# Kernel tuning notes

Hardware: AMD Instinct MI355X
Metric: run time of the kernel (lower is better)

Reference implementation:

```python
import jax, jax.numpy as jnp
import numpy as np

EMB = 2048
NH = 16
HD = EMB // NH  # 128

def setup_inputs() -> dict:
    key = jax.random.key(0)
    kx, kw1, kw2 = jax.random.split(key, 3)
    T = 4096
    x = jax.random.normal(kx, (T, EMB), dtype=jnp.float32)
    lim_in = 1.0 / np.sqrt(EMB)
    # input_proj: Linear(EMB, 3*EMB, use_bias=False), weight shape (out, in)
    W_in = jax.random.uniform(kw1, (3 * EMB, EMB), minval=-lim_in, maxval=lim_in, dtype=jnp.float32)
    W_out = jax.random.uniform(kw2, (EMB, EMB), minval=-lim_in, maxval=lim_in, dtype=jnp.float32)
    return {"x": x, "W_in": W_in, "W_out": W_out}

def reference(x, W_in, W_out):
    T = x.shape[0]
    norm = 1.0 / np.sqrt(HD)
    qkv = x @ W_in.T                         # [T, 3E]
    Q, K, V = jnp.split(qkv, 3, axis=-1)     # each [T, E]
    Q = Q.reshape(T, NH, HD).transpose(1, 0, 2)  # [nh, T, hd]
    K = K.reshape(T, NH, HD).transpose(1, 0, 2)
    V = V.reshape(T, NH, HD).transpose(1, 0, 2)
    A = jnp.einsum('htd,hsd->hts', Q, K) * norm  # [nh, T, T]
    mask = jnp.tri(T, dtype=bool)                # causal: keep lower triangle
    A = jnp.where(mask, A, -jnp.inf)
    P = jax.nn.softmax(A, axis=-1)
    y = jnp.einsum('hts,hsd->htd', P, V)         # [nh, T, hd]
    y = y.transpose(1, 0, 2).reshape(T, EMB)     # concat heads
    return y @ W_out.T
```

## Files before the change

### kernel.cpp

```cpp
#include <hip/hip_runtime.h>
#include <hip/hip_bf16.h>
#include <cstddef>


typedef __attribute__((ext_vector_type(8))) short short8;
typedef __attribute__((ext_vector_type(4))) float f32x4;

#define MFMA16(a, b, c) __builtin_amdgcn_mfma_f32_16x16x32_bf16((a), (b), (c), 0, 0, 0)

#define GLOAD_LDS16(gptr, lptr)                                                          \
  __builtin_amdgcn_global_load_lds((const __attribute__((address_space(1))) void*)(gptr), \
                                   (__attribute__((address_space(3))) void*)(lptr), 16, 0, 0)

__device__ __forceinline__ short f2bf(float f) {
  __hip_bfloat16 h = __float2bfloat16(f);
  return *reinterpret_cast<short*>(&h);
}

__device__ __forceinline__ void storeC(float* p, float v) { *p = v; }
__device__ __forceinline__ void storeC(short* p, float v) { *p = f2bf(v); }

__global__ void cvt_bf16(const float* __restrict__ in, short* __restrict__ out, long n) {
  long i = ((long)blockIdx.x * 256 + threadIdx.x) * 8;
  if (i >= n) return;
  f32x4 a = *(const f32x4*)(in + i);
  f32x4 b = *(const f32x4*)(in + i + 4);
  short8 o;
  o[0] = f2bf(a[0]); o[1] = f2bf(a[1]); o[2] = f2bf(a[2]); o[3] = f2bf(a[3]);
  o[4] = f2bf(b[0]); o[5] = f2bf(b[1]); o[6] = f2bf(b[2]); o[7] = f2bf(b[3]);
  *(short8*)(out + i) = o;
}

template <typename CT>
__global__ __launch_bounds__(256, 2)
void gemm_bt(const short* __restrict__ A, const short* __restrict__ B,
             CT* __restrict__ C, int M, int N, int K, float cscale, int nscale) {
  __shared__ short As[128 * 32];
  __shared__ short Bs[128 * 32];
  const int tid = threadIdx.x;
  const int wave = tid >> 6, lane = tid & 63;
  const int g = lane >> 4, fr = lane & 15;
  const int wr = (wave >> 1) * 64, wc = (wave & 1) * 64;
  const int bm = blockIdx.y * 128, bn = blockIdx.x * 128;

  f32x4 acc[4][4] = {};

  for (int k0 = 0; k0 < K; k0 += 32) {
    __syncthreads();
#pragma unroll
    for (int i = 0; i < 2; ++i) {
      int Ci = i * 256 + tid;
      int row = Ci >> 2, c = Ci & 3;
      int sc = c ^ (row & 3);
      GLOAD_LDS16(A + (size_t)(bm + row) * K + k0 + sc * 8, As + Ci * 8);
      GLOAD_LDS16(B + (size_t)(bn + row) * K + k0 + sc * 8, Bs + Ci * 8);
    }
    __syncthreads();

    short8 af[4], bfr[4];
#pragma unroll
    for (int m = 0; m < 4; ++m) {
      int row = wr + m * 16 + fr;
      int off = (g * 8) ^ ((row & 3) * 8);
      af[m] = *(const short8*)(As + row * 32 + off);
    }
#pragma unroll
    for (int n = 0; n < 4; ++n) {
      int row = wc + n * 16 + fr;
      int off = (g * 8) ^ ((row & 3) * 8);
      bfr[n] = *(const short8*)(Bs + row * 32 + off);
    }
#pragma unroll
    for (int m = 0; m < 4; ++m)
#pragma unroll
      for (int n = 0; n < 4; ++n)
        acc[m][n] = MFMA16(af[m], bfr[n], acc[m][n]);
  }

#pragma unroll
  for (int m = 0; m < 4; ++m) {
#pragma unroll
    for (int r = 0; r < 4; ++r) {
      size_t row = (size_t)(bm + wr + m * 16 + g * 4 + r);
      CT* cp = C + row * N + bn + wc + fr;
#pragma unroll
      for (int n = 0; n < 4; ++n) {
        float sc = (bn + wc + n * 16 + fr < nscale) ? cscale : 1.0f;
        storeC(cp + n * 16, acc[m][n][r] * sc);
      }
    }
  }
}

__global__ __launch_bounds__(256, 4)
void vtrans(const short* __restrict__ qkv, short* __restrict__ vtg) {
  __shared__ short L[128 * 64];
  const int tid = threadIdx.x;
  const int tb = blockIdx.x * 64;
  const int h = blockIdx.y;
#pragma unroll
  for (int i = 0; i < 4; ++i) {
    int Ci = i * 256 + tid, tok = Ci >> 4, c = Ci & 15, f0 = c * 8;
    short8 v = *(const short8*)(qkv + (size_t)(tb + tok) * 6144 + 4096 + h * 128 + f0);
#pragma unroll
    for (int j = 0; j < 8; ++j) {
      int f = f0 + j;
      L[f * 64 + (tok ^ ((((f & 7) ^ ((f >> 3) & 7)) << 3)))] = v[j];
    }
  }
  __syncthreads();
  const int f = tid >> 1, half = (tid & 1) * 32;
  const int s_in = ((f & 7) ^ ((f >> 3) & 7)) << 3;
  const int s_out = (f & 7) << 3;
#pragma unroll
  for (int j2 = 0; j2 < 4; ++j2) {
    int t0 = half + j2 * 8;
    short8 v = *(const short8*)(&L[f * 64 + (t0 ^ s_in)]);
    *(short8*)(vtg + (size_t)(h * 128 + f) * 4096 + tb + (t0 ^ s_out)) = v;
  }
}

__global__ __launch_bounds__(256, 1)
void attn_fwd(const short* __restrict__ qkv, const short* __restrict__ vtg,
              short* __restrict__ y) {
  __shared__ short Ks[2][64 * 128];
  __shared__ short Vt[2][128 * 64];
  __shared__ short Ps[4][32 * 72];
  const int tid = threadIdx.x;
  const int wave = tid >> 6, lane = tid & 63;
  const int g = lane >> 4, fr = lane & 15;

  const int wgid = blockIdx.x;
  const int slot = wgid >> 3;
  const int h = ((wgid & 7) << 1) | (slot >> 4);
  const int pair = slot & 15;

  short* Pw = Ps[wave];

  short8 onesf;
#pragma unroll
  for (int j = 0; j < 8; ++j) onesf[j] = (short)0x3F80;

#pragma unroll 1
  for (int phase = 0; phase < 2; ++phase) {
    const int xb = phase ? (31 - pair) : pair;
    const int qw = xb * 128 + wave * 32;
    const int ntiles = 2 * xb + 2;

    short8 qf[2][4];
#pragma unroll
    for (int mi = 0; mi < 2; ++mi) {
      const short* Qp = qkv + (size_t)(qw + mi * 16 + fr) * 6144 + h * 128;
#pragma unroll
      for (int kk = 0; kk < 4; ++kk)
        qf[mi][kk] = *(const short8*)(Qp + kk * 32 + g * 8);
    }
    f32x4 oacc[2][8] = {};
    f32x4 lacc[2] = {};

#pragma unroll
    for (int i = 0; i < 4; ++i) {
      int Ci = i * 256 + tid, key = Ci >> 4, c = Ci & 15, sc = c ^ (key & 7);
      GLOAD_LDS16(qkv + (size_t)key * 6144 + 2048 + h * 128 + sc * 8, &Ks[0][Ci * 8]);
    }
#pragma unroll
    for (int i = 0; i < 4; ++i) {
      int Ci = i * 256 + tid, feat = Ci >> 3, ko = (Ci & 7) * 8;
      GLOAD_LDS16(vtg + (size_t)(h * 128 + feat) * 4096 + ko, &Vt[0][Ci * 8]);
    }
    __syncthreads();

#pragma unroll 1
    for (int t = 0; t < ntiles; ++t) {
      const int kv0 = t * 64;
      const int cur = t & 1;

      if (t + 1 < ntiles) {
#pragma unroll
        for (int i = 0; i < 4; ++i) {
          int Ci = i * 256 + tid, key = Ci >> 4, c = Ci & 15, sc = c ^ (key & 7);
          GLOAD_LDS16(qkv + (size_t)(kv0 + 64 + key) * 6144 + 2048 + h * 128 + sc * 8,
                      &Ks[cur ^ 1][Ci * 8]);
        }
#pragma unroll
        for (int i = 0; i < 4; ++i) {
          int Ci = i * 256 + tid, feat = Ci >> 3, ko = (Ci & 7) * 8;
          GLOAD_LDS16(vtg + (size_t)(h * 128 + feat) * 4096 + kv0 + 64 + ko,
                      &Vt[cur ^ 1][Ci * 8]);
        }
      }

      f32x4 s[2][4] = {};
      __builtin_amdgcn_s_setprio(1);
#pragma unroll
      for (int nf = 0; nf < 4; ++nf) {
        const int key = nf * 16 + fr;
#pragma unroll
        for (int kk = 0; kk < 4; ++kk) {
          int off = (kk * 32 + g * 8) ^ ((key & 7) * 8);
          short8 kfrag = *(const short8*)(&Ks[cur][key * 128 + off]);
          s[0][nf] = MFMA16(qf[0][kk], kfrag, s[0][nf]);
          s[1][nf] = MFMA16(qf[1][kk], kfrag, s[1][nf]);
        }
      }
      __builtin_amdgcn_s_setprio(0);

      if (t >= ntiles - 2) {
#pragma unroll
        for (int mi = 0; mi < 2; ++mi)
#pragma unroll
          for (int nf = 0; nf < 4; ++nf) {
            const int keyg = kv0 + nf * 16 + fr;
#pragma unroll
            for (int r = 0; r < 4; ++r) {
              const int q2 = mi * 16 + g * 4 + r;
              float p = (keyg <= qw + q2) ? __builtin_amdgcn_exp2f(s[mi][nf][r]) : 0.f;
              Pw[q2 * 72 + ((nf * 16 + fr) ^ (((q2 >> 3) & 3) << 3))] = f2bf(p);
            }
          }
      } else {
#pragma unroll
        for (int mi = 0; mi < 2; ++mi)
#pragma unroll
          for (int nf = 0; nf < 4; ++nf)
#pragma unroll
            for (int r = 0; r < 4; ++r) {
              const int q2 = mi * 16 + g * 4 + r;
              Pw[q2 * 72 + ((nf * 16 + fr) ^ (((q2 >> 3) & 3) << 3))] =
                  f2bf(__builtin_amdgcn_exp2f(s[mi][nf][r]));
            }
      }

      __builtin_amdgcn_s_setprio(1);
#pragma unroll
      for (int kk = 0; kk < 2; ++kk) {
        const int rb = kk * 32 + g * 8;
        short8 pf0 = *(const short8*)(&Pw[fr * 72 + (rb ^ ((fr >> 3) << 3))]);
        short8 pf1 = *(const short8*)(&Pw[(16 + fr) * 72 + (rb ^ ((2 + (fr >> 3)) << 3))]);
        lacc[0] = MFMA16(pf0, onesf, lacc[0]);
        lacc[1] = MFMA16(pf1, onesf, lacc[1]);
#pragma unroll
        for (int nf = 0; nf < 8; ++nf) {
          int f = nf * 16 + fr;
          short8 vf = *(const short8*)(&Vt[cur][f * 64 + (rb ^ ((f & 7) * 8))]);
          oacc[0][nf] = MFMA16(pf0, vf, oacc[0][nf]);
          oacc[1][nf] = MFMA16(pf1, vf, oacc[1][nf]);
        }
      }
      __builtin_amdgcn_s_setprio(0);

      __syncthreads();
    }

#pragma unroll
    for (int mi = 0; mi < 2; ++mi)
#pragma unroll
      for (int r = 0; r < 4; ++r) {
        float inv = 1.0f / lacc[mi][r];
        size_t row = (size_t)(qw + mi * 16 + g * 4 + r);
#pragma unroll
        for (int nf = 0; nf < 8; ++nf)
          y[row * 2048 + h * 128 + nf * 16 + fr] = f2bf(oacc[mi][nf][r] * inv);
      }
  }
}

extern "C" void kernel_launch(void* const* d_in, const int* in_sizes, int n_in,
                              void* d_out, int out_size, void* d_ws, size_t ws_size,
                              hipStream_t stream) {
  const float* x    = (const float*)d_in[0];
  const float* Win  = (const float*)d_in[1];
  const float* Wout = (const float*)d_in[2];
  float* out = (float*)d_out;

  char* ws = (char*)d_ws;
  short* xb    = (short*)(ws);
  short* yb    = (short*)(ws);
  short* Winb  = (short*)(ws + 16777216);
  short* vtg   = (short*)(ws + 16777216);
  short* Woutb = (short*)(ws + 41943040);
  short* qkv   = (short*)(ws + 50331648);

  cvt_bf16<<<4096, 256, 0, stream>>>(x, xb, 8388608L);
  cvt_bf16<<<6144, 256, 0, stream>>>(Win, Winb, 12582912L);
  cvt_bf16<<<2048, 256, 0, stream>>>(Wout, Woutb, 4194304L);

  const float qscale = 0.08838834764831845f * 1.4426950408889634f;
  gemm_bt<short><<<dim3(48, 32), 256, 0, stream>>>(xb, Winb, qkv, 4096, 6144, 2048,
                                                   qscale, 2048);

  vtrans<<<dim3(64, 16), 256, 0, stream>>>(qkv, vtg);

  attn_fwd<<<256, 256, 0, stream>>>(qkv, vtg, yb);

  gemm_bt<float><<<dim3(16, 32), 256, 0, stream>>>(yb, Woutb, out, 4096, 2048, 2048,
                                                   1.0f, 0);
}
```

Before: 333.2 us.

## Fold Q scale into weight conversion, shrink P LDS, raise attention occupancy

The softmax/log2e scale for Q is now applied to the first third of W_in during bf16 conversion, so the GEMM epilogue no longer does a per-element column compare and multiply. The per-wave P scratch buffer drops its row padding (72 to 64) and uses an XOR swizzle instead to avoid bank conflicts. This shrinks LDS per block, and the attention kernel's launch bound is raised to 2 blocks per CU. The 2-block bound may force register spilling, and scaling weights before rounding to bf16 changes rounding slightly.

```diff
diff --git a/kernel.cpp b/kernel.cpp
--- a/kernel.cpp
+++ b/kernel.cpp
@@ -12,6 +12,8 @@
   __builtin_amdgcn_global_load_lds((const __attribute__((address_space(1))) void*)(gptr), \
                                    (__attribute__((address_space(3))) void*)(lptr), 16, 0, 0)
 
+#define PSWZ(q) ((((q) & 7) ^ ((q) >> 3)) << 3)
+
 __device__ __forceinline__ short f2bf(float f) {
   __hip_bfloat16 h = __float2bfloat16(f);
   return *reinterpret_cast<short*>(&h);
@@ -20,21 +22,23 @@
 __device__ __forceinline__ void storeC(float* p, float v) { *p = v; }
 __device__ __forceinline__ void storeC(short* p, float v) { *p = f2bf(v); }
 
-__global__ void cvt_bf16(const float* __restrict__ in, short* __restrict__ out, long n) {
+__global__ void cvt_bf16(const float* __restrict__ in, short* __restrict__ out,
+                         long n, float scale, long scaleN) {
   long i = ((long)blockIdx.x * 256 + threadIdx.x) * 8;
   if (i >= n) return;
+  float s = (i < scaleN) ? scale : 1.0f;
   f32x4 a = *(const f32x4*)(in + i);
   f32x4 b = *(const f32x4*)(in + i + 4);
   short8 o;
-  o[0] = f2bf(a[0]); o[1] = f2bf(a[1]); o[2] = f2bf(a[2]); o[3] = f2bf(a[3]);
-  o[4] = f2bf(b[0]); o[5] = f2bf(b[1]); o[6] = f2bf(b[2]); o[7] = f2bf(b[3]);
+  o[0] = f2bf(a[0] * s); o[1] = f2bf(a[1] * s); o[2] = f2bf(a[2] * s); o[3] = f2bf(a[3] * s);
+  o[4] = f2bf(b[0] * s); o[5] = f2bf(b[1] * s); o[6] = f2bf(b[2] * s); o[7] = f2bf(b[3] * s);
   *(short8*)(out + i) = o;
 }
 
 template <typename CT>
 __global__ __launch_bounds__(256, 2)
 void gemm_bt(const short* __restrict__ A, const short* __restrict__ B,
-             CT* __restrict__ C, int M, int N, int K, float cscale, int nscale) {
+             CT* __restrict__ C, int M, int N, int K) {
   __shared__ short As[128 * 32];
   __shared__ short Bs[128 * 32];
   const int tid = threadIdx.x;
@@ -84,10 +88,8 @@
       size_t row = (size_t)(bm + wr + m * 16 + g * 4 + r);
       CT* cp = C + row * N + bn + wc + fr;
 #pragma unroll
-      for (int n = 0; n < 4; ++n) {
-        float sc = (bn + wc + n * 16 + fr < nscale) ? cscale : 1.0f;
-        storeC(cp + n * 16, acc[m][n][r] * sc);
-      }
+      for (int n = 0; n < 4; ++n)
+        storeC(cp + n * 16, acc[m][n][r]);
     }
   }
 }
@@ -120,12 +122,12 @@
   }
 }
 
-__global__ __launch_bounds__(256, 1)
+__global__ __launch_bounds__(256, 2)
 void attn_fwd(const short* __restrict__ qkv, const short* __restrict__ vtg,
               short* __restrict__ y) {
   __shared__ short Ks[2][64 * 128];
   __shared__ short Vt[2][128 * 64];
-  __shared__ short Ps[4][32 * 72];
+  __shared__ short Ps[4][32 * 64];
   const int tid = threadIdx.x;
   const int wave = tid >> 6, lane = tid & 63;
   const int g = lane >> 4, fr = lane & 15;
@@ -215,7 +217,7 @@
             for (int r = 0; r < 4; ++r) {
               const int q2 = mi * 16 + g * 4 + r;
               float p = (keyg <= qw + q2) ? __builtin_amdgcn_exp2f(s[mi][nf][r]) : 0.f;
-              Pw[q2 * 72 + ((nf * 16 + fr) ^ (((q2 >> 3) & 3) << 3))] = f2bf(p);
+              Pw[q2 * 64 + ((nf * 16 + fr) ^ PSWZ(q2))] = f2bf(p);
             }
           }
       } else {
@@ -226,7 +228,7 @@
 #pragma unroll
             for (int r = 0; r < 4; ++r) {
               const int q2 = mi * 16 + g * 4 + r;
-              Pw[q2 * 72 + ((nf * 16 + fr) ^ (((q2 >> 3) & 3) << 3))] =
+              Pw[q2 * 64 + ((nf * 16 + fr) ^ PSWZ(q2))] =
                   f2bf(__builtin_amdgcn_exp2f(s[mi][nf][r]));
             }
       }
@@ -235,8 +237,8 @@
 #pragma unroll
       for (int kk = 0; kk < 2; ++kk) {
         const int rb = kk * 32 + g * 8;
-        short8 pf0 = *(const short8*)(&Pw[fr * 72 + (rb ^ ((fr >> 3) << 3))]);
-        short8 pf1 = *(const short8*)(&Pw[(16 + fr) * 72 + (rb ^ ((2 + (fr >> 3)) << 3))]);
+        short8 pf0 = *(const short8*)(&Pw[fr * 64 + (rb ^ PSWZ(fr))]);
+        short8 pf1 = *(const short8*)(&Pw[(16 + fr) * 64 + (rb ^ PSWZ(16 + fr))]);
         lacc[0] = MFMA16(pf0, onesf, lacc[0]);
         lacc[1] = MFMA16(pf1, onesf, lacc[1]);
 #pragma unroll
@@ -281,18 +283,17 @@
   short* Woutb = (short*)(ws + 41943040);
   short* qkv   = (short*)(ws + 50331648);
 
-  cvt_bf16<<<4096, 256, 0, stream>>>(x, xb, 8388608L);
-  cvt_bf16<<<6144, 256, 0, stream>>>(Win, Winb, 12582912L);
-  cvt_bf16<<<2048, 256, 0, stream>>>(Wout, Woutb, 4194304L);
-
   const float qscale = 0.08838834764831845f * 1.4426950408889634f;
-  gemm_bt<short><<<dim3(48, 32), 256, 0, stream>>>(xb, Winb, qkv, 4096, 6144, 2048,
-                                                   qscale, 2048);
+
+  cvt_bf16<<<4096, 256, 0, stream>>>(x, xb, 8388608L, 1.0f, 0L);
+  cvt_bf16<<<6144, 256, 0, stream>>>(Win, Winb, 12582912L, qscale, 4194304L);
+  cvt_bf16<<<2048, 256, 0, stream>>>(Wout, Woutb, 4194304L, 1.0f, 0L);
+
+  gemm_bt<short><<<dim3(48, 32), 256, 0, stream>>>(xb, Winb, qkv, 4096, 6144, 2048);
 
   vtrans<<<dim3(64, 16), 256, 0, stream>>>(qkv, vtg);
 
   attn_fwd<<<256, 256, 0, stream>>>(qkv, vtg, yb);
 
-  gemm_bt<float><<<dim3(16, 32), 256, 0, stream>>>(yb, Woutb, out, 4096, 2048, 2048,
-                                                   1.0f, 0);
-}
+  gemm_bt<float><<<dim3(16, 32), 256, 0, stream>>>(yb, Woutb, out, 4096, 2048, 2048);
+}
```

Result: slower. 341.1 us (+2.4%).
